# Kernel tuning notes

Measured on AMD Instinct MI355X. Metric: run time of the kernel, lower is better.

The kernel has to match this reference:

```python
import jax, jax.numpy as jnp
import numpy as np

SQ2PI = 0.79788456
M, D_IN, H1, H2, D_OUT = 256, 784, 256, 256, 10


def setup_inputs() -> dict:
    key = jax.random.key(0)
    ks = jax.random.split(key, 6)
    x = jax.random.normal(ks[0], (M, D_IN), dtype=jnp.float32)
    target = jax.random.randint(ks[1], (M,), 0, D_OUT)

    def init_w(k, fan_in, fan_out):
        # torch init: uniform(-1/sqrt(size(1)), 1/sqrt(size(1))) * scale (scale=1)
        stdv = 1.0 / np.sqrt(fan_out)
        return jax.random.uniform(k, (fan_in, fan_out), jnp.float32, -stdv, stdv)

    w0 = init_w(ks[2], D_IN, H1)
    w1 = init_w(ks[3], H1, H2)
    w2 = init_w(ks[4], H2, H2)
    wlast = init_w(ks[5], H2, D_OUT)
    th0 = jnp.zeros((1, H1), jnp.float32)
    th1 = jnp.zeros((1, H2), jnp.float32)
    th2 = jnp.zeros((1, H2), jnp.float32)
    thlast = jnp.zeros((1, D_OUT), jnp.float32)
    return dict(x=x, target=target, w0=w0, w1=w1, w2=w2, wlast=wlast,
                th0=th0, th1=th1, th2=th2, thlast=thlast)


def _mvg_layer(xbar, xcov, m, th):
    # sigma[b] = m^T @ xcov[b] @ m + diag(sum_j 1 - m[j,:]^2)
    s = jnp.sum(1.0 - m ** 2, axis=0)                      # [H2]
    t = jnp.einsum('bjk,kl->bjl', xcov, m)                 # [B,H,H2]
    sigma = jnp.einsum('ji,bjl->bil', m, t) + jnp.diag(s)[None]  # [B,H2,H2]
    diagsig = jnp.diagonal(sigma, axis1=1, axis2=2)        # [B,H2]
    hbar = xbar @ m + th                                   # [B,H2]
    xbar_next = jnp.tanh(SQ2PI * hbar / jnp.sqrt(diagsig))
    c = (1.0 - xbar_next ** 2) / jnp.sqrt(diagsig)         # [B,H2]
    eye = jnp.eye(m.shape[1], dtype=xbar.dtype)
    xcov_next = (SQ2PI * sigma * c[:, :, None] * c[:, None, :]
                 + eye[None] * (1.0 - xbar_next[:, None, :] ** 2))
    return xbar_next, xcov_next


def reference(x, target, w0, w1, w2, wlast, th0, th1, th2, thlast):
    m0 = 2.0 * jax.nn.sigmoid(w0) - 1.0
    m1 = 2.0 * jax.nn.sigmoid(w1) - 1.0
    m2 = 2.0 * jax.nn.sigmoid(w2) - 1.0
    mlast = 2.0 * jax.nn.sigmoid(wlast) - 1.0

    # first layer: xcov for input is implicitly zero, sigma is diagonal
    diagsig1 = jnp.sum(1.0 - m0 ** 2, axis=0)              # [H1]
    h1bar = x @ m0 + th0                                   # [M,H1]
    x1bar = jnp.tanh(SQ2PI * h1bar / jnp.sqrt(diagsig1))
    eye1 = jnp.eye(m0.shape[1], dtype=x.dtype)
    xcov1 = eye1[None] * (1.0 - x1bar[:, None, :] ** 2)    # [M,H1,H1]

    x2bar, xcov2 = _mvg_layer(x1bar, xcov1, m1, th1)
    x3bar, xcov3 = _mvg_layer(x2bar, xcov2, m2, th2)

    hlastbar = x3bar @ mlast + thlast                      # [M,10]
    logprobs = jax.nn.log_softmax(hlastbar, axis=-1)
    loss = -jnp.mean(jnp.take_along_axis(logprobs, target[:, None], axis=1))
    pred = jnp.argmax(hlastbar, axis=1)
    frac_correct = jnp.mean((pred == target).astype(jnp.float32))
    return (hlastbar, logprobs, xcov3, loss, frac_correct)
```

## Files before the change

### kernel.cpp

```cpp
#include <hip/hip_runtime.h>
#include <hip/hip_fp8.h>
#include <math.h>

#define SQ2PI_F 0.79788456f

typedef __attribute__((ext_vector_type(4))) float f32x4;
typedef __attribute__((address_space(1))) unsigned int gas_u32;
typedef __attribute__((address_space(3))) unsigned int las_u32;

__device__ inline unsigned char f2fp8(float v) { return __hip_fp8_e4m3(v).__x; }
__device__ inline float fp8tof(unsigned char b) {
  __hip_fp8_e4m3 h;
  h.__x = (__hip_fp8_storage_t)b;
  return (float)h;
}
__device__ inline unsigned int pk_fp8x4(f32x4 v) {
  return (unsigned int)f2fp8(v[0]) | ((unsigned int)f2fp8(v[1]) << 8) |
         ((unsigned int)f2fp8(v[2]) << 16) | ((unsigned int)f2fp8(v[3]) << 24);
}

__global__ void k_prep(const float* __restrict__ w0, const float* __restrict__ w1,
                       const float* __restrict__ w2, const float* __restrict__ wlast,
                       float* __restrict__ m0, float* __restrict__ m1,
                       unsigned char* __restrict__ m1f8t, float* __restrict__ m2,
                       unsigned char* __restrict__ m2f8, float* __restrict__ mlast,
                       float* __restrict__ lf) {
  int b = blockIdx.x, t = threadIdx.x;
  if (b < 784) {
    int i = b * 256 + t;
    m0[i] = tanhf(0.5f * w0[i]);
  } else if (b < 1040) {
    int j = b - 784;
    float v = tanhf(0.5f * w1[j * 256 + t]);
    m1[j * 256 + t] = v;
    m1f8t[t * 256 + j] = f2fp8(v);
  } else if (b < 1296) {
    int j = b - 1040;
    float v = tanhf(0.5f * w2[j * 256 + t]);
    m2[j * 256 + t] = v;
    m2f8[t * 256 + j] = f2fp8(v);
  } else {
    int i = (b - 1296) * 256 + t;
    if (i < 2560) mlast[i] = tanhf(0.5f * wlast[i]);
    if (b == 1296 && t < 2) lf[t] = 0.f;
  }
}

__global__ void k_layers(const float* __restrict__ x, const float* __restrict__ m0,
                         const float* __restrict__ m1, const float* __restrict__ m2,
                         const float* __restrict__ th0, const float* __restrict__ th1,
                         const float* __restrict__ th2,
                         float* __restrict__ d1g, float* __restrict__ c2,
                         float* __restrict__ d2p, float* __restrict__ h3bar,
                         float* __restrict__ s1g, float* __restrict__ s2g) {
  __shared__ float xr[784];
  __shared__ float pa[256], pb[256], pc[256];
  __shared__ float sx1[256], sd1[256], sx2[256];
  int r = blockIdx.x, t = threadIdx.x;
  int i = t & 255, h = t >> 8;
  for (int p = t; p < 784; p += 512) xr[p] = x[r * 784 + p];
  __syncthreads();
  {
    float acch = 0.f, accd = 0.f;
    int k0 = h * 392, k1 = k0 + 392;
#pragma unroll 8
    for (int k = k0; k < k1; ++k) {
      float mm = m0[k * 256 + i];
      acch = fmaf(xr[k], mm, acch);
      accd = fmaf(-mm, mm, accd + 1.f);
    }
    if (h) { pa[i] = acch; pb[i] = accd; }
    __syncthreads();
    if (!h) {
      acch += pa[i];
      accd += pb[i];
      float rs = rsqrtf(accd);
      float xb = tanhf(SQ2PI_F * (acch + th0[i]) * rs);
      float d = 1.f - xb * xb;
      sx1[i] = xb;
      sd1[i] = d;
      d1g[r * 256 + i] = d;
    }
    __syncthreads();
  }
  {
    float accd = 0.f, acch = 0.f, accs = 0.f;
    int j0 = h * 128, j1 = j0 + 128;
    for (int j = j0; j < j1; ++j) {
      float mm = m1[j * 256 + i];
      accd = fmaf(sd1[j] * mm, mm, accd);
      acch = fmaf(sx1[j], mm, acch);
      accs = fmaf(-mm, mm, accs + 1.f);
    }
    if (h) { pa[i] = accd; pb[i] = acch; pc[i] = accs; }
    __syncthreads();
    if (!h) {
      accd += pa[i];
      acch += pb[i];
      accs += pc[i];
      float rs = rsqrtf(accd + accs);
      float xb = tanhf(SQ2PI_F * (acch + th1[i]) * rs);
      float d = 1.f - xb * xb;
      c2[r * 256 + i] = d * rs;
      d2p[r * 256 + i] = d;
      sx2[i] = xb;
      if (r == 0) s1g[i] = accs;
    }
    __syncthreads();
  }
  {
    float acc3 = 0.f, acc2 = 0.f;
    int j0 = h * 128, j1 = j0 + 128;
    for (int j = j0; j < j1; ++j) {
      float mm = m2[j * 256 + i];
      acc3 = fmaf(sx2[j], mm, acc3);
      acc2 = fmaf(-mm, mm, acc2 + 1.f);
    }
    if (h) { pa[i] = acc3; pb[i] = acc2; }
    __syncthreads();
    if (!h) {
      h3bar[r * 256 + i] = acc3 + pa[i] + th2[i];
      if (r == 0) s2g[i] = acc2 + pb[i];
    }
  }
}

__global__ __launch_bounds__(1024, 4) void k_fused(
    const unsigned char* __restrict__ m1f8t, const unsigned char* __restrict__ m2f8,
    const float* __restrict__ d1, const float* __restrict__ c2,
    const float* __restrict__ d2p, const float* __restrict__ s1,
    const float* __restrict__ s2, const float* __restrict__ h3bar,
    float* __restrict__ x3bar, float* __restrict__ xcov3) {
  __shared__ __align__(16) unsigned char m2L[65536];
  __shared__ __align__(16) unsigned char XC[65536];
  __shared__ __align__(16) unsigned char SB[2][8192];
  __shared__ float c2L[256], d2pL[256], s1L[256], s2L[256];
  __shared__ float dsig[256], c3L[256], d3L[256];

  const int b = blockIdx.x;
  const int tid = threadIdx.x;
  const int l = tid & 63, w = tid >> 6;
  const int lr = l & 15, lk = l >> 4;
  const int R = w * 16;

#define PRD8(S, p, kc) \
  (*(const long*)((const unsigned char*)(S) + ((p) << 8) + ((((kc) ^ (((p) & 7) << 1))) << 3)))
#define SWZ32(p, j0) (((p) << 8) + ((((j0) >> 3) ^ (((p) & 7) << 1)) << 3) + ((j0) & 7))

#pragma unroll
  for (int q = 0; q < 4; ++q) {
    int rl = q * 64 + w * 4 + (l >> 4);
    int c = l & 15;
    const unsigned char* src = m2f8 + rl * 256 + ((c ^ (rl & 7)) << 4);
    unsigned char* dst = m2L + (q * 64 + w * 4) * 256;
    __builtin_amdgcn_global_load_lds((const gas_u32*)src, (las_u32*)dst, 16, 0, 0);
  }
  if (w < 8) {
    int rl = w * 4 + (l >> 4);
    int c = l & 15;
    const unsigned char* src = m1f8t + rl * 256 + ((c ^ (rl & 7)) << 4);
    __builtin_amdgcn_global_load_lds((const gas_u32*)src,
                                     (las_u32*)(SB[0] + (w * 4) * 256), 16, 0, 0);
  }

  if (tid < 256) {
    c2L[tid] = c2[b * 256 + tid];
    d2pL[tid] = d2p[b * 256 + tid];
    s1L[tid] = s1[tid];
    s2L[tid] = s2[tid];
    dsig[tid] = 0.f;
  }

  const float* d1b = d1 + b * 256;

  long af_w[8];
#pragma unroll
  for (int ks = 0; ks < 8; ++ks) {
    unsigned long long mr =
        *(const unsigned long long*)(m1f8t + (size_t)(R + lr) * 256 + ks * 32 + lk * 8);
    const float* dp = d1b + ks * 32 + lk * 8;
    unsigned long long out = 0;
#pragma unroll
    for (int e = 0; e < 8; ++e) {
      float v = fp8tof((unsigned char)(mr >> (8 * e))) * dp[e];
      out |= ((unsigned long long)f2fp8(v)) << (8 * e);
    }
    af_w[ks] = (long)out;
  }
  __syncthreads();

  long afX[8];

#pragma unroll
  for (int cp = 0; cp < 8; ++cp) {
    if (cp < 7 && w < 8) {
      int rl = w * 4 + (l >> 4);
      int c = l & 15;
      const unsigned char* src =
          m1f8t + (size_t)(cp + 1) * 8192 + rl * 256 + ((c ^ (rl & 7)) << 4);
      __builtin_amdgcn_global_load_lds(
          (const gas_u32*)src, (las_u32*)(SB[(cp + 1) & 1] + (w * 4) * 256), 16, 0, 0);
    }
    const unsigned char* sbc = SB[cp & 1];
    f32x4 acc[2];
    acc[0] = {0.f, 0.f, 0.f, 0.f};
    acc[1] = {0.f, 0.f, 0.f, 0.f};
#pragma unroll
    for (int ks = 0; ks < 8; ++ks) {
      long bq0 = PRD8(sbc, lr, ks * 4 + lk);
      long bq1 = PRD8(sbc, 16 + lr, ks * 4 + lk);
      acc[0] = __builtin_amdgcn_mfma_f32_16x16x32_fp8_fp8(af_w[ks], bq0, acc[0], 0, 0, 0);
      acc[1] = __builtin_amdgcn_mfma_f32_16x16x32_fp8_fp8(af_w[ks], bq1, acc[1], 0, 0, 0);
    }
    unsigned char* XP = XC + (cp & 1) * 8192;
    int r0 = R + lk * 4;
#pragma unroll
    for (int j = 0; j < 2; ++j) {
      int p = j * 16 + lr;
      int cc = cp * 32 + p;
      float c2c = c2L[cc];
      f32x4 st;
#pragma unroll
      for (int e = 0; e < 4; ++e) {
        int r = r0 + e;
        float g = acc[j][e];
        if (r == cc) g += s1L[r];
        float v = SQ2PI_F * c2L[r] * c2c * g;
        if (r == cc) v += d2pL[r];
        st[e] = v;
      }
      *(unsigned int*)(XP + SWZ32(p, r0)) = pk_fp8x4(st);
    }
    __syncthreads();
    if (cp == (w >> 1)) {
      int p2 = (w & 1) * 16 + lr;
#pragma unroll
      for (int ks = 0; ks < 8; ++ks) afX[ks] = PRD8(XP, p2, ks * 4 + lk);
    }
  }
  __syncthreads();

#pragma unroll
  for (int lf = 0; lf < 16; ++lf) {
    f32x4 at = {0.f, 0.f, 0.f, 0.f};
#pragma unroll
    for (int ks = 0; ks < 8; ++ks) {
      long bq = PRD8(m2L, lf * 16 + lr, ks * 4 + lk);
      at = __builtin_amdgcn_mfma_f32_16x16x32_fp8_fp8(afX[ks], bq, at, 0, 0, 0);
    }
    int j0 = R + lk * 4;
    int lq = lf * 16 + lr;
    *(unsigned int*)(XC + SWZ32(lq, j0)) = pk_fp8x4(at);
    unsigned int mraw = *(const unsigned int*)(m2L + SWZ32(lq, j0));
    float s = 0.f;
#pragma unroll
    for (int e = 0; e < 4; ++e)
      s = fmaf(fp8tof((unsigned char)(mraw >> (8 * e))), at[e], s);
    s += __shfl_xor(s, 16, 64);
    s += __shfl_xor(s, 32, 64);
    if (lk == 0) atomicAdd(&dsig[lq], s);
  }
  __syncthreads();

  if (tid < 256) {
    float ds = dsig[tid] + s2L[tid];
    float rs = rsqrtf(ds);
    float xb = tanhf(SQ2PI_F * h3bar[b * 256 + tid] * rs);
    x3bar[b * 256 + tid] = xb;
    float d = 1.f - xb * xb;
    c3L[tid] = d * rs;
    d3L[tid] = d;
  }
  __syncthreads();

  long am2[8];
#pragma unroll
  for (int ks = 0; ks < 8; ++ks) am2[ks] = PRD8(m2L, R + lr, ks * 4 + lk);

#pragma unroll
  for (int lf = 0; lf < 16; ++lf) {
    f32x4 sc = {0.f, 0.f, 0.f, 0.f};
    int p = lf * 16 + lr;
#pragma unroll
    for (int ks = 0; ks < 8; ++ks) {
      long bq = PRD8(XC, p, ks * 4 + lk);
      sc = __builtin_amdgcn_mfma_f32_16x16x32_fp8_fp8(am2[ks], bq, sc, 0, 0, 0);
    }
    int i0 = R + lk * 4;
    int gl = p;
    float cg = c3L[gl];
    f32x4 st;
#pragma unroll
    for (int e = 0; e < 4; ++e) {
      int i = i0 + e;
      float g = sc[e];
      if (i == gl) g += s2L[i];
      float v = SQ2PI_F * c3L[i] * cg * g;
      if (i == gl) v += d3L[i];
      st[e] = v;
    }
    *(f32x4*)(xcov3 + ((size_t)b << 16) + (size_t)gl * 256 + i0) = st;
  }
#undef PRD8
#undef SWZ32
}

__global__ void k_final4(const float* __restrict__ x3bar, const float* __restrict__ mlast,
                         const float* __restrict__ thlast, const int* __restrict__ target,
                         float* __restrict__ hlast_out, float* __restrict__ logp_out,
                         float* __restrict__ loss_out, float* __restrict__ frac_out) {
  __shared__ float Wl[2560];
  int t = threadIdx.x;
  int r = blockIdx.x * 64 + t;
  for (int p = t; p < 2560; p += 64) Wl[p] = mlast[p];
  __syncthreads();
  float acc[10];
#pragma unroll
  for (int c = 0; c < 10; ++c) acc[c] = thlast[c];
  for (int j = 0; j < 256; ++j) {
    float xv = x3bar[r * 256 + j];
#pragma unroll
    for (int c = 0; c < 10; ++c) acc[c] = fmaf(xv, Wl[j * 10 + c], acc[c]);
  }
#pragma unroll
  for (int c = 0; c < 10; ++c) hlast_out[r * 10 + c] = acc[c];
  float mx = acc[0];
  int am = 0;
#pragma unroll
  for (int c = 1; c < 10; ++c)
    if (acc[c] > mx) { mx = acc[c]; am = c; }
  float se = 0.f;
#pragma unroll
  for (int c = 0; c < 10; ++c) se += expf(acc[c] - mx);
  float lse = logf(se);
#pragma unroll
  for (int c = 0; c < 10; ++c) logp_out[r * 10 + c] = acc[c] - mx - lse;
  int tg = target[r];
  float lossc = -(acc[tg] - mx - lse) * (1.f / 256.f);
  float corr = (am == tg) ? (1.f / 256.f) : 0.f;
#pragma unroll
  for (int off = 32; off > 0; off >>= 1) {
    lossc += __shfl_down(lossc, off);
    corr += __shfl_down(corr, off);
  }
  if (t == 0) {
    atomicAdd(loss_out, lossc);
    atomicAdd(frac_out, corr);
  }
}


extern "C" void kernel_launch(void* const* d_in, const int* in_sizes, int n_in,
                              void* d_out, int out_size, void* d_ws, size_t ws_size,
                              hipStream_t stream) {
  const float* x = (const float*)d_in[0];
  const int* target = (const int*)d_in[1];
  const float* w0 = (const float*)d_in[2];
  const float* w1 = (const float*)d_in[3];
  const float* w2 = (const float*)d_in[4];
  const float* wlast = (const float*)d_in[5];
  const float* th0 = (const float*)d_in[6];
  const float* th1 = (const float*)d_in[7];
  const float* th2 = (const float*)d_in[8];
  const float* thlast = (const float*)d_in[9];

  float* W = (float*)d_ws;
  size_t o = 0;
  auto alloc = [&](size_t n) { float* p = W + o; o += n; return p; };
  float* m0 = alloc(200704);
  float* m1 = alloc(65536);
  float* m2 = alloc(65536);
  float* mlast = alloc(2560);
  float* s1 = alloc(256);
  float* s2 = alloc(256);
  float* d1 = alloc(65536);
  float* c2 = alloc(65536);
  float* d2p = alloc(65536);
  float* h3bar = alloc(65536);
  float* x3bar = alloc(65536);
  unsigned char* m1f8t = (unsigned char*)alloc(16384);
  unsigned char* m2f8 = (unsigned char*)alloc(16384);

  float* hlast = (float*)d_out;
  float* logp = hlast + 2560;
  float* xcov3_out = logp + 2560;
  float* loss = xcov3_out + 16777216;
  float* frac = loss + 1;

  k_prep<<<1306, 256, 0, stream>>>(w0, w1, w2, wlast, m0, m1, m1f8t, m2, m2f8,
                                   mlast, loss);
  k_layers<<<256, 512, 0, stream>>>(x, m0, m1, m2, th0, th1, th2, d1, c2, d2p,
                                    h3bar, s1, s2);
  k_fused<<<256, 1024, 0, stream>>>(m1f8t, m2f8, d1, c2, d2p, s1, s2,
                                    h3bar, x3bar, xcov3_out);
  k_final4<<<4, 64, 0, stream>>>(x3bar, mlast, thlast, target, hlast, logp, loss, frac);
}
```

Measured before the change: 129.4 us.

## Retile fused MFMA stages to 32x16 warp tiles and use hardware fp8 conversions

Each wave now owns a 32-row by 16-column tile (two A fragments sharing one B fragment) instead of 16 rows across all columns. This halves the LDS B-fragment reads per MFMA in all three GEMM stages and halves the loop trip counts. It also replaces the software fp8 encode/decode with the packed hardware convert builtins and vectorises the d1 loads. In exchange it doubles the A-fragment register arrays, which raises register pressure under the 1024-thread launch bound.

```diff
diff --git a/kernel.cpp b/kernel.cpp
--- a/kernel.cpp
+++ b/kernel.cpp
@@ -8,15 +8,42 @@
 typedef __attribute__((address_space(1))) unsigned int gas_u32;
 typedef __attribute__((address_space(3))) unsigned int las_u32;
 
+#if defined(__has_builtin)
+#if __has_builtin(__builtin_amdgcn_cvt_pk_fp8_f32) && __has_builtin(__builtin_amdgcn_cvt_f32_fp8)
+#define HW_FP8 1
+#endif
+#endif
+
 __device__ inline unsigned char f2fp8(float v) { return __hip_fp8_e4m3(v).__x; }
-__device__ inline float fp8tof(unsigned char b) {
-  __hip_fp8_e4m3 h;
-  h.__x = (__hip_fp8_storage_t)b;
-  return (float)h;
-}
+
 __device__ inline unsigned int pk_fp8x4(f32x4 v) {
+#ifdef HW_FP8
+  int r = 0;
+  r = __builtin_amdgcn_cvt_pk_fp8_f32(v[0], v[1], r, false);
+  r = __builtin_amdgcn_cvt_pk_fp8_f32(v[2], v[3], r, true);
+  return (unsigned int)r;
+#else
   return (unsigned int)f2fp8(v[0]) | ((unsigned int)f2fp8(v[1]) << 8) |
          ((unsigned int)f2fp8(v[2]) << 16) | ((unsigned int)f2fp8(v[3]) << 24);
+#endif
+}
+
+__device__ inline f32x4 upk_fp8x4(unsigned int r) {
+  f32x4 o;
+#ifdef HW_FP8
+  o[0] = __builtin_amdgcn_cvt_f32_fp8((int)r, 0);
+  o[1] = __builtin_amdgcn_cvt_f32_fp8((int)r, 1);
+  o[2] = __builtin_amdgcn_cvt_f32_fp8((int)r, 2);
+  o[3] = __builtin_amdgcn_cvt_f32_fp8((int)r, 3);
+#else
+  __hip_fp8_e4m3 h;
+#pragma unroll
+  for (int e = 0; e < 4; ++e) {
+    h.__x = (__hip_fp8_storage_t)((r >> (8 * e)) & 0xff);
+    o[e] = (float)h;
+  }
+#endif
+  return o;
 }
 
 __global__ void k_prep(const float* __restrict__ w0, const float* __restrict__ w1,
@@ -141,7 +168,8 @@
   const int tid = threadIdx.x;
   const int l = tid & 63, w = tid >> 6;
   const int lr = l & 15, lk = l >> 4;
-  const int R = w * 16;
+  const int wr = w >> 1, wc = w & 1;
+  const int R32 = wr * 32;
 
 #define PRD8(S, p, kc) \
   (*(const long*)((const unsigned char*)(S) + ((p) << 8) + ((((kc) ^ (((p) & 7) << 1))) << 3)))
@@ -173,23 +201,30 @@
 
   const float* d1b = d1 + b * 256;
 
-  long af_w[8];
-#pragma unroll
-  for (int ks = 0; ks < 8; ++ks) {
-    unsigned long long mr =
-        *(const unsigned long long*)(m1f8t + (size_t)(R + lr) * 256 + ks * 32 + lk * 8);
-    const float* dp = d1b + ks * 32 + lk * 8;
-    unsigned long long out = 0;
-#pragma unroll
-    for (int e = 0; e < 8; ++e) {
-      float v = fp8tof((unsigned char)(mr >> (8 * e))) * dp[e];
-      out |= ((unsigned long long)f2fp8(v)) << (8 * e);
-    }
-    af_w[ks] = (long)out;
-  }
-  __syncthreads();
-
-  long afX[8];
+  long af_w[16];
+#pragma unroll
+  for (int f = 0; f < 2; ++f) {
+#pragma unroll
+    for (int ks = 0; ks < 8; ++ks) {
+      unsigned long long mr = *(const unsigned long long*)(
+          m1f8t + (size_t)(R32 + f * 16 + lr) * 256 + ks * 32 + lk * 8);
+      f32x4 w0 = upk_fp8x4((unsigned int)mr);
+      f32x4 w1 = upk_fp8x4((unsigned int)(mr >> 32));
+      f32x4 dv0 = *(const f32x4*)(d1b + ks * 32 + lk * 8);
+      f32x4 dv1 = *(const f32x4*)(d1b + ks * 32 + lk * 8 + 4);
+      f32x4 v0, v1;
+#pragma unroll
+      for (int e = 0; e < 4; ++e) {
+        v0[e] = w0[e] * dv0[e];
+        v1[e] = w1[e] * dv1[e];
+      }
+      unsigned long long o0 = pk_fp8x4(v0), o1 = pk_fp8x4(v1);
+      af_w[f * 8 + ks] = (long)((o1 << 32) | o0);
+    }
+  }
+  __syncthreads();
+
+  long afX[16];
 
 #pragma unroll
   for (int cp = 0; cp < 8; ++cp) {
@@ -202,63 +237,70 @@
           (const gas_u32*)src, (las_u32*)(SB[(cp + 1) & 1] + (w * 4) * 256), 16, 0, 0);
     }
     const unsigned char* sbc = SB[cp & 1];
-    f32x4 acc[2];
-    acc[0] = {0.f, 0.f, 0.f, 0.f};
-    acc[1] = {0.f, 0.f, 0.f, 0.f};
+    const int p = wc * 16 + lr;
+    f32x4 acc0 = {0.f, 0.f, 0.f, 0.f};
+    f32x4 acc1 = {0.f, 0.f, 0.f, 0.f};
 #pragma unroll
     for (int ks = 0; ks < 8; ++ks) {
-      long bq0 = PRD8(sbc, lr, ks * 4 + lk);
-      long bq1 = PRD8(sbc, 16 + lr, ks * 4 + lk);
-      acc[0] = __builtin_amdgcn_mfma_f32_16x16x32_fp8_fp8(af_w[ks], bq0, acc[0], 0, 0, 0);
-      acc[1] = __builtin_amdgcn_mfma_f32_16x16x32_fp8_fp8(af_w[ks], bq1, acc[1], 0, 0, 0);
+      long bq = PRD8(sbc, p, ks * 4 + lk);
+      acc0 = __builtin_amdgcn_mfma_f32_16x16x32_fp8_fp8(af_w[ks], bq, acc0, 0, 0, 0);
+      acc1 = __builtin_amdgcn_mfma_f32_16x16x32_fp8_fp8(af_w[8 + ks], bq, acc1, 0, 0, 0);
     }
     unsigned char* XP = XC + (cp & 1) * 8192;
-    int r0 = R + lk * 4;
-#pragma unroll
-    for (int j = 0; j < 2; ++j) {
-      int p = j * 16 + lr;
-      int cc = cp * 32 + p;
-      float c2c = c2L[cc];
+    const int cc = cp * 32 + p;
+    const float c2c = c2L[cc];
+#pragma unroll
+    for (int f = 0; f < 2; ++f) {
+      int j0 = R32 + f * 16 + lk * 4;
+      f32x4 ac = f ? acc1 : acc0;
       f32x4 st;
 #pragma unroll
       for (int e = 0; e < 4; ++e) {
-        int r = r0 + e;
-        float g = acc[j][e];
+        int r = j0 + e;
+        float g = ac[e];
         if (r == cc) g += s1L[r];
         float v = SQ2PI_F * c2L[r] * c2c * g;
         if (r == cc) v += d2pL[r];
         st[e] = v;
       }
-      *(unsigned int*)(XP + SWZ32(p, r0)) = pk_fp8x4(st);
-    }
-    __syncthreads();
-    if (cp == (w >> 1)) {
-      int p2 = (w & 1) * 16 + lr;
-#pragma unroll
-      for (int ks = 0; ks < 8; ++ks) afX[ks] = PRD8(XP, p2, ks * 4 + lk);
-    }
-  }
-  __syncthreads();
-
-#pragma unroll
-  for (int lf = 0; lf < 16; ++lf) {
-    f32x4 at = {0.f, 0.f, 0.f, 0.f};
+      *(unsigned int*)(XP + SWZ32(p, j0)) = pk_fp8x4(st);
+    }
+    __syncthreads();
+    if (cp == wr) {
+#pragma unroll
+      for (int ks = 0; ks < 8; ++ks) {
+        afX[ks] = PRD8(XP, lr, ks * 4 + lk);
+        afX[8 + ks] = PRD8(XP, 16 + lr, ks * 4 + lk);
+      }
+    }
+  }
+  __syncthreads();
+
+#pragma unroll
+  for (int lf = 0; lf < 8; ++lf) {
+    const int p = wc * 128 + lf * 16 + lr;
+    f32x4 at0 = {0.f, 0.f, 0.f, 0.f};
+    f32x4 at1 = {0.f, 0.f, 0.f, 0.f};
 #pragma unroll
     for (int ks = 0; ks < 8; ++ks) {
-      long bq = PRD8(m2L, lf * 16 + lr, ks * 4 + lk);
-      at = __builtin_amdgcn_mfma_f32_16x16x32_fp8_fp8(afX[ks], bq, at, 0, 0, 0);
-    }
-    int j0 = R + lk * 4;
-    int lq = lf * 16 + lr;
-    *(unsigned int*)(XC + SWZ32(lq, j0)) = pk_fp8x4(at);
-    unsigned int mraw = *(const unsigned int*)(m2L + SWZ32(lq, j0));
+      long bq = PRD8(m2L, p, ks * 4 + lk);
+      at0 = __builtin_amdgcn_mfma_f32_16x16x32_fp8_fp8(afX[ks], bq, at0, 0, 0, 0);
+      at1 = __builtin_amdgcn_mfma_f32_16x16x32_fp8_fp8(afX[8 + ks], bq, at1, 0, 0, 0);
+    }
+    const int j0 = R32 + lk * 4;
+    *(unsigned int*)(XC + SWZ32(p, j0)) = pk_fp8x4(at0);
+    *(unsigned int*)(XC + SWZ32(p, j0 + 16)) = pk_fp8x4(at1);
+    f32x4 mv0 = upk_fp8x4(*(const unsigned int*)(m2L + SWZ32(p, j0)));
+    f32x4 mv1 = upk_fp8x4(*(const unsigned int*)(m2L + SWZ32(p, j0 + 16)));
     float s = 0.f;
 #pragma unroll
-    for (int e = 0; e < 4; ++e)
-      s = fmaf(fp8tof((unsigned char)(mraw >> (8 * e))), at[e], s);
+    for (int e = 0; e < 4; ++e) {
+      s = fmaf(mv0[e], at0[e], s);
+      s = fmaf(mv1[e], at1[e], s);
+    }
     s += __shfl_xor(s, 16, 64);
     s += __shfl_xor(s, 32, 64);
-    if (lk == 0) atomicAdd(&dsig[lq], s);
+    if (lk == 0) atomicAdd(&dsig[p], s);
   }
   __syncthreads();
 
@@ -273,33 +315,42 @@
   }
   __syncthreads();
 
-  long am2[8];
-#pragma unroll
-  for (int ks = 0; ks < 8; ++ks) am2[ks] = PRD8(m2L, R + lr, ks * 4 + lk);
-
-#pragma unroll
-  for (int lf = 0; lf < 16; ++lf) {
-    f32x4 sc = {0.f, 0.f, 0.f, 0.f};
-    int p = lf * 16 + lr;
+  long am2[16];
+#pragma unroll
+  for (int f = 0; f < 2; ++f)
+#pragma unroll
+    for (int ks = 0; ks < 8; ++ks)
+      am2[f * 8 + ks] = PRD8(m2L, R32 + f * 16 + lr, ks * 4 + lk);
+
+#pragma unroll
+  for (int lf = 0; lf < 8; ++lf) {
+    const int p = wc * 128 + lf * 16 + lr;
+    f32x4 sc0 = {0.f, 0.f, 0.f, 0.f};
+    f32x4 sc1 = {0.f, 0.f, 0.f, 0.f};
 #pragma unroll
     for (int ks = 0; ks < 8; ++ks) {
       long bq = PRD8(XC, p, ks * 4 + lk);
-      sc = __builtin_amdgcn_mfma_f32_16x16x32_fp8_fp8(am2[ks], bq, sc, 0, 0, 0);
-    }
-    int i0 = R + lk * 4;
-    int gl = p;
-    float cg = c3L[gl];
-    f32x4 st;
-#pragma unroll
-    for (int e = 0; e < 4; ++e) {
-      int i = i0 + e;
-      float g = sc[e];
-      if (i == gl) g += s2L[i];
-      float v = SQ2PI_F * c3L[i] * cg * g;
-      if (i == gl) v += d3L[i];
-      st[e] = v;
-    }
-    *(f32x4*)(xcov3 + ((size_t)b << 16) + (size_t)gl * 256 + i0) = st;
+      sc0 = __builtin_amdgcn_mfma_f32_16x16x32_fp8_fp8(am2[ks], bq, sc0, 0, 0, 0);
+      sc1 = __builtin_amdgcn_mfma_f32_16x16x32_fp8_fp8(am2[8 + ks], bq, sc1, 0, 0, 0);
+    }
+    const int gl = p;
+    const float cg = c3L[gl];
+#pragma unroll
+    for (int f = 0; f < 2; ++f) {
+      int i0 = R32 + f * 16 + lk * 4;
+      f32x4 sc = f ? sc1 : sc0;
+      f32x4 st;
+#pragma unroll
+      for (int e = 0; e < 4; ++e) {
+        int i = i0 + e;
+        float g = sc[e];
+        if (i == gl) g += s2L[i];
+        float v = SQ2PI_F * c3L[i] * cg * g;
+        if (i == gl) v += d3L[i];
+        st[e] = v;
+      }
+      *(f32x4*)(xcov3 + ((size_t)b << 16) + (size_t)gl * 256 + i0) = st;
+    }
   }
 #undef PRD8
 #undef SWZ32
```

Result: faster. 122.5 us (-5.4%).
